# Optimization experiments

Hardware: AMD Instinct MI355X
Metric: run time of the kernel (lower is better)

## Reference

```python
import jax, jax.numpy as jnp
import numpy as np

GH, GW, H, B, IN = 4, 2, 512, 8192, 1
FC_HID = H // 2
NC = GH * GW
BN_EPS = 1e-5


def setup_inputs() -> dict:
    key = jax.random.key(0)
    ks = jax.random.split(key, 20)
    def n(k, shape, s=1.0):
        return jax.random.normal(k, shape, dtype=jnp.float32) * s
    return {
        "x": n(ks[0], (B, GH, GW)),
        "h_ext": n(ks[1], (B, H), 0.1),
        "c_ext": n(ks[2], (B, H), 0.1),
        "grid_h": n(ks[3], (GH, GW, B, H), 0.1),
        "grid_c": n(ks[4], (GH, GW, B, H), 0.1),
        "Wh": n(ks[5], (NC, H, 3 * H), (3 * H) ** -0.5),
        "bh": n(ks[6], (NC, H), 0.01),
        "Wc": n(ks[7], (NC, H, 3 * H), (3 * H) ** -0.5),
        "bc": n(ks[8], (NC, H), 0.01),
        "W_ih": n(ks[9], (NC, 4 * H, IN), 1.0),
        "W_hh": n(ks[10], (NC, 4 * H, H), H ** -0.5),
        "b_ih": n(ks[11], (NC, 4 * H), 0.01),
        "b_hh": n(ks[12], (NC, 4 * H), 0.01),
        "W1": n(ks[13], (FC_HID, 2 * H), (2 * H) ** -0.5),
        "b1": n(ks[14], (FC_HID,), 0.01),
        "W2": n(ks[15], (1, FC_HID), FC_HID ** -0.5),
        "b2": n(ks[16], (1,), 0.01),
        "gamma": jnp.ones((1,), jnp.float32),
        "beta": jnp.zeros((1,), jnp.float32),
    }


def _lattice_forward(x, h_ext, c_ext, grid_h, grid_c, Wh, bh, Wc, bc,
                     W_ih, W_hh, b_ih, b_hh, W1, b1, W2, b2, gamma, beta):
    b = x.shape[0]
    zeros = jnp.zeros((b, H), x.dtype)
    # python lists over the small fixed 4x2 grid (strict left/up dependency)
    sh = [[grid_h[i, j] for j in range(GW)] for i in range(GH)]
    sc = [[grid_c[i, j] for j in range(GW)] for i in range(GH)]
    for i in range(GH):
        for j in range(GW):
            k = i * GW + j
            h_prev, c_prev = sh[i][j], sc[i][j]
            if i == 0 and j == 0:
                h_left, c_left = h_ext, c_ext
            elif j > 0:
                h_left, c_left = sh[i][j - 1], sc[i][j - 1]
            else:
                h_left, c_left = zeros, zeros
            if i > 0:
                h_up, c_up = sh[i - 1][j], sc[i - 1][j]
            else:
                h_up, c_up = zeros, zeros
            comb_h = jnp.concatenate([h_left, h_up, h_prev], axis=1)  # [B,3H]
            comb_c = jnp.concatenate([c_left, c_up, c_prev], axis=1)
            ph = comb_h @ Wh[k].T + bh[k]  # [B,H]
            pc = comb_c @ Wc[k].T + bc[k]
            xi = x[:, i, j][:, None]  # [B,1]
            gates = xi @ W_ih[k].T + b_ih[k] + ph @ W_hh[k].T + b_hh[k]  # [B,4H]
            ig, fg, gg, og = jnp.split(gates, 4, axis=1)
            c_new = jax.nn.sigmoid(fg) * pc + jax.nn.sigmoid(ig) * jnp.tanh(gg)
            h_new = jax.nn.sigmoid(og) * jnp.tanh(c_new)
            sh[i][j], sc[i][j] = h_new, c_new
    final_h = sh[-1][-1] + h_ext
    final_c = sc[-1][-1] + c_ext
    final = jnp.concatenate([final_h, final_c], axis=1)  # [B,2H]
    hid = jax.nn.relu(final @ W1.T + b1)
    out = hid @ W2.T + b2  # [B,1]
    # BatchNorm1d in training mode: biased batch stats over the batch dim
    mu = jnp.mean(out, axis=0, keepdims=True)
    var = jnp.mean((out - mu) ** 2, axis=0, keepdims=True)
    out = gamma * (out - mu) * jax.lax.rsqrt(var + BN_EPS) + beta
    out = jax.nn.sigmoid(out)
    new_gh = jnp.stack([jnp.stack(row) for row in sh])  # [GH,GW,B,H]
    new_gc = jnp.stack([jnp.stack(row) for row in sc])
    return out, final_h, final_c, new_gh, new_gc


def reference(x, h_ext, c_ext, grid_h, grid_c, Wh, bh, Wc, bc,
              W_ih, W_hh, b_ih, b_hh, W1, b1, W2, b2, gamma, beta):
    return _lattice_forward(x, h_ext, c_ext, grid_h, grid_c, Wh, bh, Wc, bc,
                            W_ih, W_hh, b_ih, b_hh, W1, b1, W2, b2, gamma, beta)
```

## Files before the change

### kernel.cpp

```cpp
#include <hip/hip_runtime.h>
#include <stdint.h>

#define B_SZ 8192
static const size_t BH = (size_t)B_SZ * 512;

typedef short bfrag8 __attribute__((ext_vector_type(8)));
typedef float f32x4 __attribute__((ext_vector_type(4)));

__device__ __forceinline__ unsigned short f2bf(float f) {
  union { float f; uint32_t u; } c; c.f = f;
  uint32_t u = c.u;
  uint32_t r = (u + 0x7FFFu + ((u >> 16) & 1u)) >> 16;
  return (unsigned short)r;
}
__device__ __forceinline__ float bf2f(unsigned short u) {
  union { uint32_t u; float f; } c; c.u = ((uint32_t)u) << 16;
  return c.f;
}
__device__ __forceinline__ uint32_t pk2(float a, float b) {
  uint32_t r;
  asm("v_cvt_pk_bf16_f32 %0, %1, %2" : "=v"(r) : "v"(a), "v"(b));
  return r;
}
__device__ __forceinline__ float sigm(float x) { return 1.0f / (1.0f + __expf(-x)); }
__device__ __forceinline__ float tanh_fast(float x) {
  float cx = fminf(fmaxf(x, -15.0f), 15.0f);
  float e = __expf(2.0f * cx);
  return (e - 1.0f) / (e + 1.0f);
}

__device__ __forceinline__ void gload16(const void* g, void* l) {
  __builtin_amdgcn_global_load_lds(
      (const __attribute__((address_space(1))) void*)g,
      (__attribute__((address_space(3))) void*)l, 16, 0, 0);
}

__device__ __forceinline__ void xcd_swizzle(int& bx, int& by, int& bz) {
  int nx = gridDim.x, ny = gridDim.y, nz = gridDim.z;
  int nwg = nx * ny * nz;
  int id = blockIdx.x + nx * (blockIdx.y + ny * blockIdx.z);
  int q = nwg >> 3, r = nwg & 7;
  int xcd = id & 7, lin = id >> 3;
  int swz = (xcd < r ? xcd * (q + 1) : r * (q + 1) + (xcd - r) * q) + lin;
  bx = swz % nx; swz /= nx;
  by = swz % ny; bz = swz / ny;
}

struct P8Job {
  const float* A[3];
  int co[3];
  int nseg;
  const unsigned short* B;
  const float* bias;
  unsigned short* outBf;
};
struct P8Args {
  P8Job j[4];
  int ldB, outStride;
};

__global__ __launch_bounds__(512, 1) void pgemm256_k(P8Args pa) {
  extern __shared__ char lds[];
  int bx, by, bz;
  xcd_swizzle(bx, by, bz);
  const P8Job jb = pa.j[bz];
  const int tid = threadIdx.x;
  const int lane = tid & 63;
  const int wv = tid >> 6;
  const int wr = wv >> 2, wc = wv & 3;
  const int m0 = by * 256;

  int rowS[4], cgS[4];
  const char* bPtr[4];
#pragma unroll
  for (int q = 0; q < 4; ++q) {
    int cl = q * 512 + tid;
    int row = cl >> 3, cs = cl & 7;
    cgS[q] = cs ^ (row & 7);
    rowS[q] = row;
    bPtr[q] = (const char*)jb.B + (size_t)(bx * 256 + row) * pa.ldB * 2;
  }

  auto loadA = [&](int t, float4* a0, float4* a1) {
    int seg = t >> 3, k0 = (t & 7) << 6;
    const float* Ab = jb.A[seg];
#pragma unroll
    for (int q = 0; q < 4; ++q) {
      const float4* p = (const float4*)(Ab + (size_t)(m0 + rowS[q]) * 512 + k0 +
                                        cgS[q] * 8);
      a0[q] = p[0];
      a1[q] = p[1];
    }
  };
  auto stageB = [&](int t, int buf) {
    int seg = t >> 3, k0 = (t & 7) << 6;
    int coB = (jb.co[seg] + k0) * 2;
    char* Bb = lds + 65536 + buf * 32768;
#pragma unroll
    for (int q = 0; q < 4; ++q)
      gload16(bPtr[q] + coB + cgS[q] * 16, Bb + (q * 512 + tid) * 16);
  };
  auto writeA = [&](const float4* a0, const float4* a1, int buf) {
    char* Ab = lds + buf * 32768;
#pragma unroll
    for (int q = 0; q < 4; ++q) {
      uint4 w;
      w.x = pk2(a0[q].x, a0[q].y);
      w.y = pk2(a0[q].z, a0[q].w);
      w.z = pk2(a1[q].x, a1[q].y);
      w.w = pk2(a1[q].z, a1[q].w);
      *(uint4*)(Ab + (q * 512 + tid) * 16) = w;
    }
  };

  f32x4 acc[8][4];
#pragma unroll
  for (int a = 0; a < 8; ++a)
#pragma unroll
    for (int b = 0; b < 4; ++b) acc[a][b] = f32x4{0.f, 0.f, 0.f, 0.f};

  const int nt = jb.nseg * 8;

  {
    float4 a0[4], a1[4];
    loadA(0, a0, a1);
    stageB(0, 0);
    writeA(a0, a1, 0);
  }
  __syncthreads();

  int cur = 0;
  for (int t = 0; t < nt; ++t) {
    float4 a0[4], a1[4];
    const bool more = (t + 1 < nt);
    if (more) {
      loadA(t + 1, a0, a1);
      stageB(t + 1, cur ^ 1);
    }
    const char* As = lds + cur * 32768;
    const char* Bs = lds + 65536 + cur * 32768;
    bfrag8 bfr[4][2];
#pragma unroll
    for (int nf = 0; nf < 4; ++nf)
#pragma unroll
      for (int ks = 0; ks < 2; ++ks) {
        int row = wc * 64 + nf * 16 + (lane & 15);
        bfr[nf][ks] = *(const bfrag8*)(Bs + row * 128 +
                                       (((ks * 4 + (lane >> 4)) ^ (row & 7)) * 16));
      }
#pragma unroll
    for (int mf = 0; mf < 8; ++mf) {
      bfrag8 af[2];
#pragma unroll
      for (int ks = 0; ks < 2; ++ks) {
        int row = wr * 128 + mf * 16 + (lane & 15);
        af[ks] = *(const bfrag8*)(As + row * 128 +
                                  (((ks * 4 + (lane >> 4)) ^ (row & 7)) * 16));
      }
#pragma unroll
      for (int nf = 0; nf < 4; ++nf)
#pragma unroll
        for (int ks = 0; ks < 2; ++ks)
          acc[mf][nf] = __builtin_amdgcn_mfma_f32_16x16x32_bf16(
              af[ks], bfr[nf][ks], acc[mf][nf], 0, 0, 0);
    }
    if (more) writeA(a0, a1, cur ^ 1);
    __syncthreads();
    cur ^= 1;
  }

  const int c4 = lane & 15;
  const int r4 = lane >> 4;
  const int n0 = bx * 256;
#pragma unroll
  for (int nf = 0; nf < 4; ++nf) {
    int colg = n0 + wc * 64 + nf * 16 + c4;
    float bv = jb.bias[colg];
#pragma unroll
    for (int mf = 0; mf < 8; ++mf)
#pragma unroll
      for (int r = 0; r < 4; ++r) {
        int rowg = m0 + wr * 128 + mf * 16 + r4 * 4 + r;
        jb.outBf[(size_t)rowg * pa.outStride + colg] = f2bf(acc[mf][nf][r] + bv);
      }
  }
}

__global__ __launch_bounds__(512, 1) void pgemm128_k(P8Args pa) {
  extern __shared__ char lds[];
  int bx, by, bz;
  xcd_swizzle(bx, by, bz);
  const P8Job jb = pa.j[bz];
  const int tid = threadIdx.x;
  const int lane = tid & 63;
  const int wv = tid >> 6;
  const int wr = wv >> 2, wc = wv & 3;
  const int m0 = by * 128;

  int cgB[4];
  const char* bPtr[4];
#pragma unroll
  for (int q = 0; q < 4; ++q) {
    int cl = q * 512 + tid;
    int row = cl >> 3, cs = cl & 7;
    cgB[q] = cs ^ (row & 7);
    bPtr[q] = (const char*)jb.B + (size_t)(bx * 256 + row) * pa.ldB * 2;
  }
  int rowA[2], cgA[2];
#pragma unroll
  for (int q = 0; q < 2; ++q) {
    int cl = q * 512 + tid;
    int row = cl >> 3, cs = cl & 7;
    cgA[q] = cs ^ (row & 7);
    rowA[q] = row;
  }

  auto stageB = [&](int t, int buf) {
    int seg = t >> 3, k0 = (t & 7) << 6;
    int coB = (jb.co[seg] + k0) * 2;
    char* Bb = lds + 32768 + buf * 32768;
#pragma unroll
    for (int q = 0; q < 4; ++q)
      gload16(bPtr[q] + coB + cgB[q] * 16, Bb + (q * 512 + tid) * 16);
  };
  auto loadA = [&](int t, float4* a0, float4* a1) {
    int seg = t >> 3, k0 = (t & 7) << 6;
    const float* Ab = jb.A[seg];
#pragma unroll
    for (int q = 0; q < 2; ++q) {
      const float4* p = (const float4*)(Ab + (size_t)(m0 + rowA[q]) * 512 + k0 +
                                        cgA[q] * 8);
      a0[q] = p[0];
      a1[q] = p[1];
    }
  };
  auto writeA = [&](const float4* a0, const float4* a1, int buf) {
    char* Ab = lds + buf * 16384;
#pragma unroll
    for (int q = 0; q < 2; ++q) {
      uint4 w;
      w.x = pk2(a0[q].x, a0[q].y);
      w.y = pk2(a0[q].z, a0[q].w);
      w.z = pk2(a1[q].x, a1[q].y);
      w.w = pk2(a1[q].z, a1[q].w);
      *(uint4*)(Ab + (q * 512 + tid) * 16) = w;
    }
  };

  f32x4 acc[4][4];
#pragma unroll
  for (int a = 0; a < 4; ++a)
#pragma unroll
    for (int b = 0; b < 4; ++b) acc[a][b] = f32x4{0.f, 0.f, 0.f, 0.f};

  const int nt = jb.nseg * 8;

  {
    float4 a0[2], a1[2];
    stageB(0, 0);
    loadA(0, a0, a1);
    writeA(a0, a1, 0);
  }
  __syncthreads();

  int cur = 0;
  for (int t = 0; t < nt; ++t) {
    float4 a0[2], a1[2];
    const bool more = (t + 1 < nt);
    if (more) {
      stageB(t + 1, cur ^ 1);
      loadA(t + 1, a0, a1);
    }
    const char* As = lds + cur * 16384;
    const char* Bs = lds + 32768 + cur * 32768;
    bfrag8 bfr[4][2];
#pragma unroll
    for (int nf = 0; nf < 4; ++nf)
#pragma unroll
      for (int ks = 0; ks < 2; ++ks) {
        int row = wc * 64 + nf * 16 + (lane & 15);
        bfr[nf][ks] = *(const bfrag8*)(Bs + row * 128 +
                                       (((ks * 4 + (lane >> 4)) ^ (row & 7)) * 16));
      }
#pragma unroll
    for (int mf = 0; mf < 4; ++mf) {
      bfrag8 af[2];
#pragma unroll
      for (int ks = 0; ks < 2; ++ks) {
        int row = wr * 64 + mf * 16 + (lane & 15);
        af[ks] = *(const bfrag8*)(As + row * 128 +
                                  (((ks * 4 + (lane >> 4)) ^ (row & 7)) * 16));
      }
#pragma unroll
      for (int nf = 0; nf < 4; ++nf)
#pragma unroll
        for (int ks = 0; ks < 2; ++ks)
          acc[mf][nf] = __builtin_amdgcn_mfma_f32_16x16x32_bf16(
              af[ks], bfr[nf][ks], acc[mf][nf], 0, 0, 0);
    }
    if (more) writeA(a0, a1, cur ^ 1);
    __syncthreads();
    cur ^= 1;
  }

  const int c4 = lane & 15;
  const int r4 = lane >> 4;
  const int n0 = bx * 256;
#pragma unroll
  for (int nf = 0; nf < 4; ++nf) {
    int colg = n0 + wc * 64 + nf * 16 + c4;
    float bv = jb.bias[colg];
#pragma unroll
    for (int mf = 0; mf < 4; ++mf)
#pragma unroll
      for (int r = 0; r < 4; ++r) {
        int rowg = m0 + wr * 64 + mf * 16 + r4 * 4 + r;
        jb.outBf[(size_t)rowg * pa.outStride + colg] = f2bf(acc[mf][nf][r] + bv);
      }
  }
}

struct GJob {
  const unsigned short* ph;
  const unsigned short* Whh;
  const unsigned short* pc;
  float* gh; float* gc;
  int cell, last;
};
struct GArgs {
  GJob j[2];
  const float* x;
  const float* W_ih; const float* b_ih; const float* b_hh;
  const float* h_ext; const float* c_ext;
  float* fh; float* fc;
  unsigned short* finalB;
};

__global__ __launch_bounds__(512, 2) void gates_k(GArgs ga) {
  extern __shared__ char lds[];
  int bx, by, bz;
  xcd_swizzle(bx, by, bz);
  const GJob jb = ga.j[bz];
  const int tid = threadIdx.x;
  const int lane = tid & 63;
  const int wv = tid >> 6;
  const int wr = wv >> 2;
  const int wc = wv & 3;
  const int m0 = by * 256;

  int rowS[4], cgS[4];
  const char* bPtr[4];
#pragma unroll
  for (int q = 0; q < 4; ++q) {
    int cl = q * 512 + tid;
    int row = cl >> 3, cs = cl & 7;
    cgS[q] = cs ^ (row & 7);
    rowS[q] = row;
    int browG = ((row >> 4) & 3) * 512 + bx * 64 + ((row >> 6) << 4) + (row & 15);
    bPtr[q] = (const char*)jb.Whh + (size_t)browG * 512 * 2;
  }

  auto stage = [&](int t, int buf) {
    int k0 = t << 6;
    char* Ab = lds + buf * 32768;
    char* Bb = lds + 65536 + buf * 32768;
#pragma unroll
    for (int q = 0; q < 4; ++q)
      gload16((const char*)jb.ph + ((size_t)(m0 + rowS[q]) * 512 + k0) * 2 + cgS[q] * 16,
              Ab + (q * 512 + tid) * 16);
#pragma unroll
    for (int q = 0; q < 4; ++q)
      gload16(bPtr[q] + k0 * 2 + cgS[q] * 16, Bb + (q * 512 + tid) * 16);
  };

  f32x4 acc[8][4];
#pragma unroll
  for (int a = 0; a < 8; ++a)
#pragma unroll
    for (int b = 0; b < 4; ++b) acc[a][b] = f32x4{0.f, 0.f, 0.f, 0.f};

  stage(0, 0);
  asm volatile("s_waitcnt vmcnt(0)" ::: "memory");
  __builtin_amdgcn_s_barrier();
  asm volatile("" ::: "memory");

  int cur = 0;
  for (int t = 0; t < 8; ++t) {
    if (t + 1 < 8) stage(t + 1, cur ^ 1);
    const char* As = lds + cur * 32768;
    const char* Bs = lds + 65536 + cur * 32768;
    bfrag8 bfr[4][2];
#pragma unroll
    for (int nf = 0; nf < 4; ++nf)
#pragma unroll
      for (int ks = 0; ks < 2; ++ks) {
        int row = wc * 64 + nf * 16 + (lane & 15);
        bfr[nf][ks] = *(const bfrag8*)(Bs + row * 128 +
                                       (((ks * 4 + (lane >> 4)) ^ (row & 7)) * 16));
      }
#pragma unroll
    for (int mf = 0; mf < 8; ++mf) {
      bfrag8 af[2];
#pragma unroll
      for (int ks = 0; ks < 2; ++ks) {
        int row = wr * 128 + mf * 16 + (lane & 15);
        af[ks] = *(const bfrag8*)(As + row * 128 +
                                  (((ks * 4 + (lane >> 4)) ^ (row & 7)) * 16));
      }
#pragma unroll
      for (int nf = 0; nf < 4; ++nf)
#pragma unroll
        for (int ks = 0; ks < 2; ++ks)
          acc[mf][nf] = __builtin_amdgcn_mfma_f32_16x16x32_bf16(
              af[ks], bfr[nf][ks], acc[mf][nf], 0, 0, 0);
    }
    asm volatile("s_waitcnt vmcnt(0)" ::: "memory");
    __builtin_amdgcn_s_barrier();
    asm volatile("" ::: "memory");
    cur ^= 1;
  }

  const int c4 = lane & 15;
  const int r4 = lane >> 4;
  int hcol = bx * 64 + wc * 16 + c4;
  const float* Wih = ga.W_ih + jb.cell * 2048;
  const float* bih = ga.b_ih + jb.cell * 2048;
  const float* bhh = ga.b_hh + jb.cell * 2048;
  float wih[4], gb[4];
#pragma unroll
  for (int q = 0; q < 4; ++q) {
    wih[q] = Wih[q * 512 + hcol];
    gb[q] = bih[q * 512 + hcol] + bhh[q * 512 + hcol];
  }
#pragma unroll
  for (int mf = 0; mf < 8; ++mf)
#pragma unroll
    for (int r = 0; r < 4; ++r) {
      int b = m0 + wr * 128 + mf * 16 + r4 * 4 + r;
      float xi = ga.x[b * 8 + jb.cell];
      float vi = acc[mf][0][r] + xi * wih[0] + gb[0];
      float vf = acc[mf][1][r] + xi * wih[1] + gb[1];
      float vg = acc[mf][2][r] + xi * wih[2] + gb[2];
      float vo = acc[mf][3][r] + xi * wih[3] + gb[3];
      size_t o = (size_t)b * 512 + hcol;
      float pcv = bf2f(jb.pc[o]);
      float cn = sigm(vf) * pcv + sigm(vi) * tanh_fast(vg);
      float hn = sigm(vo) * tanh_fast(cn);
      jb.gh[o] = hn;
      jb.gc[o] = cn;
      if (jb.last) {
        float fh = hn + ga.h_ext[o];
        float fc = cn + ga.c_ext[o];
        ga.fh[o] = fh;
        ga.fc[o] = fc;
        ga.finalB[(size_t)b * 1024 + hcol] = f2bf(fh);
        ga.finalB[(size_t)b * 1024 + 512 + hcol] = f2bf(fc);
      }
    }
}

struct PJob {
  const void* A[3];
  int co[3];
  int nseg, relu;
  const unsigned short* B;
  const float* bias;
  unsigned short* outBf;
};
struct PArgs {
  PJob j[8];
  int ldA, ldB, outStride;
};

__global__ __launch_bounds__(256, 4) void pgemm_k(PArgs pa) {
  __shared__ __align__(16) char As[16384];
  __shared__ __align__(16) char Bs[16384];
  int bx, by, bz;
  xcd_swizzle(bx, by, bz);
  const PJob jb = pa.j[bz];
  const int tid = threadIdx.x;
  const int lane = tid & 63;
  const int wv = tid >> 6;
  const int wr = wv >> 1, wc = wv & 1;
  const int m0 = by * 128;

  int rowA[4], cg[4];
  const char* browPtr[4];
#pragma unroll
  for (int q = 0; q < 4; ++q) {
    int cl = q * 256 + tid;
    int row = cl >> 3, cs = cl & 7;
    cg[q] = cs ^ (row & 7);
    rowA[q] = row;
    browPtr[q] = (const char*)jb.B + (size_t)(bx * 128 + row) * pa.ldB * 2;
  }

  f32x4 acc[4][4];
#pragma unroll
  for (int a = 0; a < 4; ++a)
#pragma unroll
    for (int b = 0; b < 4; ++b) acc[a][b] = f32x4{0.f, 0.f, 0.f, 0.f};

  for (int s = 0; s < jb.nseg; ++s) {
    const char* Abase = (const char*)jb.A[s];
    const int coB = jb.co[s] * 2;
    for (int k0 = 0; k0 < 512; k0 += 64) {
#pragma unroll
      for (int q = 0; q < 4; ++q)
        gload16(Abase + ((size_t)(m0 + rowA[q]) * pa.ldA + k0) * 2 + cg[q] * 16,
                As + (q * 256 + tid) * 16);
#pragma unroll
      for (int q = 0; q < 4; ++q)
        gload16(browPtr[q] + coB + k0 * 2 + cg[q] * 16,
                Bs + (q * 256 + tid) * 16);
      __syncthreads();
#pragma unroll
      for (int ks = 0; ks < 2; ++ks) {
        bfrag8 af[4], bfr[4];
#pragma unroll
        for (int mf = 0; mf < 4; ++mf) {
          int row = wr * 64 + mf * 16 + (lane & 15);
          af[mf] = *(const bfrag8*)(As + row * 128 +
                                    ((ks * 4 + (lane >> 4)) ^ (row & 7)) * 16);
        }
#pragma unroll
        for (int nf = 0; nf < 4; ++nf) {
          int row = wc * 64 + nf * 16 + (lane & 15);
          bfr[nf] = *(const bfrag8*)(Bs + row * 128 +
                                     ((ks * 4 + (lane >> 4)) ^ (row & 7)) * 16);
        }
#pragma unroll
        for (int mf = 0; mf < 4; ++mf)
#pragma unroll
          for (int nf = 0; nf < 4; ++nf)
            acc[mf][nf] = __builtin_amdgcn_mfma_f32_16x16x32_bf16(
                af[mf], bfr[nf], acc[mf][nf], 0, 0, 0);
      }
      __syncthreads();
    }
  }

  const int c4 = lane & 15;
  const int r4 = lane >> 4;
  const int n0 = bx * 128;
#pragma unroll
  for (int nf = 0; nf < 4; ++nf) {
    int colg = n0 + wc * 64 + nf * 16 + c4;
    float bv = jb.bias[colg];
#pragma unroll
    for (int mf = 0; mf < 4; ++mf)
#pragma unroll
      for (int r = 0; r < 4; ++r) {
        int rowg = m0 + wr * 64 + mf * 16 + r4 * 4 + r;
        size_t o = (size_t)rowg * pa.outStride + colg;
        float v = acc[mf][nf][r] + bv;
        if (jb.relu) v = fmaxf(v, 0.0f);
        jb.outBf[o] = f2bf(v);
      }
  }
}

struct CvtArgs {
  const float4* s[8];
  uint2* d[8];
  long start[9];
};
__global__ __launch_bounds__(256) void convert_many(CvtArgs ca) {
  long total = ca.start[8];
  long stride = (long)gridDim.x * blockDim.x;
  for (long idx = (long)blockIdx.x * blockDim.x + threadIdx.x; idx < total;
       idx += stride) {
    int jb = 0;
#pragma unroll
    for (int q = 1; q < 8; ++q) jb += (idx >= ca.start[q]) ? 1 : 0;
    long local = idx - ca.start[jb];
    float4 v = ca.s[jb][local];
    uint2 o;
    o.x = (uint32_t)f2bf(v.x) | ((uint32_t)f2bf(v.y) << 16);
    o.y = (uint32_t)f2bf(v.z) | ((uint32_t)f2bf(v.w) << 16);
    ca.d[jb][local] = o;
  }
}

__global__ __launch_bounds__(256)
void fc2_kernel(const unsigned short* hid, const float* W2, const float* b2,
                float* outlin) {
  int row = blockIdx.x * 4 + (threadIdx.x >> 6);
  int lane = threadIdx.x & 63;
  uint2 hv = ((const uint2*)(hid + (size_t)row * 256))[lane];
  float4 wv = ((const float4*)W2)[lane];
  float s = bf2f((unsigned short)(hv.x & 0xffffu)) * wv.x +
            bf2f((unsigned short)(hv.x >> 16)) * wv.y +
            bf2f((unsigned short)(hv.y & 0xffffu)) * wv.z +
            bf2f((unsigned short)(hv.y >> 16)) * wv.w;
#pragma unroll
  for (int o = 32; o > 0; o >>= 1) s += __shfl_down(s, o);
  if (lane == 0) outlin[row] = s + b2[0];
}

__global__ __launch_bounds__(1024)
void bn_kernel(const float* outlin, const float* gamma, const float* beta,
               float* out) {
  __shared__ float sred[16], sred2[16];
  __shared__ float smu, srs;
  float s = 0.f, s2 = 0.f;
  for (int i = threadIdx.x; i < 8192; i += 1024) {
    float v = outlin[i];
    s += v; s2 += v * v;
  }
#pragma unroll
  for (int o = 32; o > 0; o >>= 1) { s += __shfl_down(s, o); s2 += __shfl_down(s2, o); }
  if ((threadIdx.x & 63) == 0) { sred[threadIdx.x >> 6] = s; sred2[threadIdx.x >> 6] = s2; }
  __syncthreads();
  if (threadIdx.x == 0) {
    float S = 0.f, S2 = 0.f;
    for (int q = 0; q < 16; ++q) { S += sred[q]; S2 += sred2[q]; }
    float mu = S * (1.0f / 8192.0f);
    float var = S2 * (1.0f / 8192.0f) - mu * mu;
    smu = mu; srs = rsqrtf(var + 1e-5f);
  }
  __syncthreads();
  float gm = gamma[0], bt = beta[0];
  for (int i = threadIdx.x; i < 8192; i += 1024) {
    float v = (outlin[i] - smu) * srs * gm + bt;
    out[i] = sigm(v);
  }
}

extern "C" void kernel_launch(void* const* d_in, const int* in_sizes, int n_in,
                              void* d_out, int out_size, void* d_ws, size_t ws_size,
                              hipStream_t stream) {
  const float* x      = (const float*)d_in[0];
  const float* h_ext  = (const float*)d_in[1];
  const float* c_ext  = (const float*)d_in[2];
  const float* grid_h = (const float*)d_in[3];
  const float* grid_c = (const float*)d_in[4];
  const float* Wh     = (const float*)d_in[5];
  const float* bh     = (const float*)d_in[6];
  const float* Wc     = (const float*)d_in[7];
  const float* bc     = (const float*)d_in[8];
  const float* W_ih   = (const float*)d_in[9];
  const float* W_hh   = (const float*)d_in[10];
  const float* b_ih   = (const float*)d_in[11];
  const float* b_hh   = (const float*)d_in[12];
  const float* W1     = (const float*)d_in[13];
  const float* b1     = (const float*)d_in[14];
  const float* W2     = (const float*)d_in[15];
  const float* b2     = (const float*)d_in[16];
  const float* gamma  = (const float*)d_in[17];
  const float* beta   = (const float*)d_in[18];

  float* out = (float*)d_out;
  float* fh_out = out + 8192;
  float* fc_out = fh_out + BH;
  float* gh_out = fc_out + BH;
  float* gc_out = gh_out + 8 * BH;

  char* ws = (char*)d_ws;
  size_t off = 0;
  auto alloc = [&](size_t bytes) {
    char* p = ws + off;
    off = (off + bytes + 255) & ~(size_t)255;
    return p;
  };
  unsigned short* whB   = (unsigned short*)alloc(8ull * 512 * 1536 * 2);
  unsigned short* wcB   = (unsigned short*)alloc(8ull * 512 * 1536 * 2);
  unsigned short* whhB  = (unsigned short*)alloc(8ull * 2048 * 512 * 2);
  unsigned short* w1B   = (unsigned short*)alloc(256ull * 1024 * 2);
  unsigned short* pcB   = (unsigned short*)alloc(8 * BH * 2);
  unsigned short* phB   = (unsigned short*)alloc(8 * BH * 2);
  unsigned short* finalB = (unsigned short*)alloc((size_t)B_SZ * 1024 * 2);
  unsigned short* hidB   = (unsigned short*)alloc((size_t)B_SZ * 256 * 2);
  float*          outlin = (float*)alloc((size_t)B_SZ * 4);

  hipFuncSetAttribute((const void*)gates_k,
                      hipFuncAttributeMaxDynamicSharedMemorySize, 131072);
  hipFuncSetAttribute((const void*)pgemm256_k,
                      hipFuncAttributeMaxDynamicSharedMemorySize, 131072);
  hipFuncSetAttribute((const void*)pgemm128_k,
                      hipFuncAttributeMaxDynamicSharedMemorySize, 98304);

  {
    CvtArgs ca;
    long n4[4] = {8L * 512 * 1536 / 4, 8L * 512 * 1536 / 4,
                  8L * 2048 * 512 / 4, 256L * 1024 / 4};
    const float* srcs[4] = {Wh, Wc, W_hh, W1};
    unsigned short* dsts[4] = {whB, wcB, whhB, w1B};
    ca.start[0] = 0;
    for (int q = 0; q < 8; ++q) {
      int qq = q < 4 ? q : 3;
      ca.s[q] = (const float4*)srcs[qq];
      ca.d[q] = (uint2*)dsts[qq];
      ca.start[q + 1] = ca.start[q] + (q < 4 ? n4[q] : 0);
    }
    convert_many<<<2048, 256, 0, stream>>>(ca);
  }

  auto launch_p = [&](const int* cells, int n) {
    P8Args pa = {};
    pa.ldB = 1536; pa.outStride = 512;
    for (int q = 0; q < n; ++q) {
      int k = cells[q];
      int i = k >> 1, jj = k & 1;
      P8Job& jh = pa.j[2 * q];
      P8Job& jc = pa.j[2 * q + 1];
      jh = P8Job{}; jc = P8Job{};
      int ns = 0;
      if (k == 0) {
        jh.A[ns] = h_ext; jc.A[ns] = c_ext;
        jh.co[ns] = 0; jc.co[ns] = 0; ns++;
      } else if (jj > 0) {
        jh.A[ns] = gh_out + (size_t)(k - 1) * BH;
        jc.A[ns] = gc_out + (size_t)(k - 1) * BH;
        jh.co[ns] = 0; jc.co[ns] = 0; ns++;
      }
      if (i > 0) {
        jh.A[ns] = gh_out + (size_t)(k - 2) * BH;
        jc.A[ns] = gc_out + (size_t)(k - 2) * BH;
        jh.co[ns] = 512; jc.co[ns] = 512; ns++;
      }
      jh.A[ns] = grid_h + (size_t)k * BH;
      jc.A[ns] = grid_c + (size_t)k * BH;
      jh.co[ns] = 1024; jc.co[ns] = 1024; ns++;
      jh.nseg = ns; jc.nseg = ns;
      jh.B = whB + (size_t)k * 512 * 1536; jh.bias = bh + k * 512;
      jc.B = wcB + (size_t)k * 512 * 1536; jc.bias = bc + k * 512;
      jh.outBf = phB + (size_t)k * BH;
      jc.outBf = pcB + (size_t)k * BH;
    }
    if (n == 1)
      pgemm128_k<<<dim3(2, 64, 2), 512, 98304, stream>>>(pa);
    else
      pgemm256_k<<<dim3(2, 32, 2 * n), 512, 131072, stream>>>(pa);
  };

  auto launch_gates = [&](const int* cells, int n) {
    GArgs ga = {};
    ga.x = x; ga.W_ih = W_ih; ga.b_ih = b_ih; ga.b_hh = b_hh;
    ga.h_ext = h_ext; ga.c_ext = c_ext;
    ga.fh = fh_out; ga.fc = fc_out; ga.finalB = finalB;
    for (int q = 0; q < n; ++q) {
      int k = cells[q];
      GJob& j = ga.j[q];
      j.ph = phB + (size_t)k * BH;
      j.Whh = whhB + (size_t)k * 2048 * 512;
      j.pc = pcB + (size_t)k * BH;
      j.gh = gh_out + (size_t)k * BH;
      j.gc = gc_out + (size_t)k * BH;
      j.cell = k; j.last = (k == 7);
    }
    gates_k<<<dim3(8, 32, n), 512, 131072, stream>>>(ga);
  };

  const int diags[5][2] = {{0, -1}, {1, 2}, {3, 4}, {5, 6}, {7, -1}};
  const int dn[5] = {1, 2, 2, 2, 1};
  for (int d = 0; d < 5; ++d) {
    launch_p(diags[d], dn[d]);
    launch_gates(diags[d], dn[d]);
  }

  {
    PArgs pa = {};
    pa.ldA = 1024; pa.ldB = 1024; pa.outStride = 256;
    PJob& j = pa.j[0];
    j = PJob{};
    j.A[0] = finalB; j.co[0] = 0;
    j.A[1] = finalB + 512; j.co[1] = 512;
    j.nseg = 2; j.relu = 1;
    j.B = w1B; j.bias = b1; j.outBf = hidB;
    pgemm_k<<<dim3(2, 64, 1), 256, 0, stream>>>(pa);
  }

  fc2_kernel<<<2048, 256, 0, stream>>>(hidB, W2, b2, outlin);
  bn_kernel<<<1, 1024, 0, stream>>>(outlin, gamma, beta, out);
}
```

Baseline: 653.0 us.

## Use partial vmcnt waits so next-tile global loads overlap current MFMA compute

Replaces full __syncthreads/vmcnt(0) waits in three GEMM kernels with explicit s_waitcnt vmcnt(N) before a raw barrier at the top of each iteration. The current tile's direct-to-LDS loads can complete while the next tile's loads stay in flight, so global memory latency overlaps the MFMA loop instead of draining every iteration. This depends on the hardcoded vmcnt counts exactly matching the per-thread issue order. If they do not, the kernels race on LDS. One kernel also reorders loadA before stageB to make the counts line up.

```diff
diff --git a/kernel.cpp b/kernel.cpp
--- a/kernel.cpp
+++ b/kernel.cpp
@@ -45,6 +45,8 @@
   bx = swz % nx; swz /= nx;
   by = swz % ny; bz = swz / ny;
 }
+
+#define BARRIER() __builtin_amdgcn_s_barrier()
 
 struct P8Job {
   const float* A[3];
@@ -127,7 +129,6 @@
     stageB(0, 0);
     writeA(a0, a1, 0);
   }
-  __syncthreads();
 
   int cur = 0;
   for (int t = 0; t < nt; ++t) {
@@ -136,7 +137,12 @@
     if (more) {
       loadA(t + 1, a0, a1);
       stageB(t + 1, cur ^ 1);
-    }
+      asm volatile("s_waitcnt vmcnt(12) lgkmcnt(0)" ::: "memory");
+    } else {
+      asm volatile("s_waitcnt vmcnt(0) lgkmcnt(0)" ::: "memory");
+    }
+    BARRIER();
+    asm volatile("" ::: "memory");
     const char* As = lds + cur * 32768;
     const char* Bs = lds + 65536 + cur * 32768;
     bfrag8 bfr[4][2];
@@ -165,7 +171,9 @@
               af[ks], bfr[nf][ks], acc[mf][nf], 0, 0, 0);
     }
     if (more) writeA(a0, a1, cur ^ 1);
-    __syncthreads();
+    asm volatile("s_waitcnt lgkmcnt(0)" ::: "memory");
+    BARRIER();
+    asm volatile("" ::: "memory");
     cur ^= 1;
   }
 
@@ -261,16 +269,20 @@
     loadA(0, a0, a1);
     writeA(a0, a1, 0);
   }
-  __syncthreads();
 
   int cur = 0;
   for (int t = 0; t < nt; ++t) {
     float4 a0[2], a1[2];
     const bool more = (t + 1 < nt);
     if (more) {
+      loadA(t + 1, a0, a1);
       stageB(t + 1, cur ^ 1);
-      loadA(t + 1, a0, a1);
-    }
+      asm volatile("s_waitcnt vmcnt(8) lgkmcnt(0)" ::: "memory");
+    } else {
+      asm volatile("s_waitcnt vmcnt(0) lgkmcnt(0)" ::: "memory");
+    }
+    BARRIER();
+    asm volatile("" ::: "memory");
     const char* As = lds + cur * 16384;
     const char* Bs = lds + 32768 + cur * 32768;
     bfrag8 bfr[4][2];
@@ -299,7 +311,9 @@
               af[ks], bfr[nf][ks], acc[mf][nf], 0, 0, 0);
     }
     if (more) writeA(a0, a1, cur ^ 1);
-    __syncthreads();
+    asm volatile("s_waitcnt lgkmcnt(0)" ::: "memory");
+    BARRIER();
+    asm volatile("" ::: "memory");
     cur ^= 1;
   }
 
@@ -380,13 +394,16 @@
     for (int b = 0; b < 4; ++b) acc[a][b] = f32x4{0.f, 0.f, 0.f, 0.f};
 
   stage(0, 0);
-  asm volatile("s_waitcnt vmcnt(0)" ::: "memory");
-  __builtin_amdgcn_s_barrier();
-  asm volatile("" ::: "memory");
-
   int cur = 0;
   for (int t = 0; t < 8; ++t) {
-    if (t + 1 < 8) stage(t + 1, cur ^ 1);
+    if (t + 1 < 8) {
+      stage(t + 1, cur ^ 1);
+      asm volatile("s_waitcnt vmcnt(8)" ::: "memory");
+    } else {
+      asm volatile("s_waitcnt vmcnt(0)" ::: "memory");
+    }
+    BARRIER();
+    asm volatile("" ::: "memory");
     const char* As = lds + cur * 32768;
     const char* Bs = lds + 65536 + cur * 32768;
     bfrag8 bfr[4][2];
@@ -414,8 +431,7 @@
           acc[mf][nf] = __builtin_amdgcn_mfma_f32_16x16x32_bf16(
               af[ks], bfr[nf][ks], acc[mf][nf], 0, 0, 0);
     }
-    asm volatile("s_waitcnt vmcnt(0)" ::: "memory");
-    __builtin_amdgcn_s_barrier();
+    BARRIER();
     asm volatile("" ::: "memory");
     cur ^= 1;
   }
```

Result: no change. 665.3 us (+1.9%).
